# Kernel tuning notes

Measured on AMD Instinct MI355X. Metric: run time of the kernel, lower is better.

Reference implementation:

```python
import jax, jax.numpy as jnp
import numpy as np

MARGIN = 1.0
EPS = 1e-11


def setup_inputs() -> dict:
    key = jax.random.key(0)
    k1, k2, k3 = jax.random.split(key, 3)
    B, D, C = 8192, 512, 128
    features = jax.random.normal(k1, (B, D), dtype=jnp.float32)
    labels = jax.random.randint(k2, (B,), 0, C, dtype=jnp.int64)
    neg_u = jax.random.uniform(k3, (B,), dtype=jnp.float32)
    return {"features": features, "labels": labels, "neg_u": neg_u}


def reference(features, labels, neg_u):
    n = features.shape[0]
    sq = jnp.sum(features * features, axis=1)  # [n]
    d2 = sq[:, None] + sq[None, :] - 2.0 * (features @ features.T)
    dist = jnp.sqrt(jnp.clip(d2, EPS, None))  # [n, n]

    same = labels[:, None] == labels[None, :]
    eye = jnp.eye(n, dtype=bool)
    pos_mask = same & ~eye           # valid positives per anchor
    neg_mask = ~same                 # valid negatives per anchor
    n_neg = neg_mask.sum(axis=1)     # [n]

    # deterministic "random" negative: pick the floor(u * n_neg)-th negative
    # (stable argsort puts negatives first, preserving original order)
    order = jnp.argsort(jnp.where(neg_mask, 0, 1), axis=1, stable=True)  # [n, n]
    k = jnp.floor(neg_u * n_neg.astype(neg_u.dtype)).astype(jnp.int32)
    k = jnp.clip(k, 0, jnp.maximum(n_neg - 1, 0).astype(jnp.int32))
    neg_idx = jnp.take_along_axis(order, k[:, None], axis=1)[:, 0]       # [n]
    neg_dist = dist[jnp.arange(n), neg_idx]                               # [n]

    # MarginRankingLoss(y=1): max(0, margin + pos_dist - neg_dist), per (anchor, pos) pair
    valid = pos_mask & (n_neg > 0)[:, None]
    per_pair = jnp.maximum(MARGIN + dist - neg_dist[:, None], 0.0)
    counter = valid.sum()
    total = jnp.where(valid, per_pair, 0.0).sum()
    return total / counter.astype(total.dtype)
```

## Files before the change

kernel.cpp:

```cpp
#include <hip/hip_runtime.h>
#include <hip/hip_bf16.h>
#include <cstdint>

#define NN 8192
#define DD 512
#define NC 128

typedef unsigned short u16;
typedef __attribute__((ext_vector_type(8))) short short8;
typedef __attribute__((ext_vector_type(4))) float f32x4;

#define AS1 __attribute__((address_space(1)))
#define AS3 __attribute__((address_space(3)))

#define FB_OFF   ((size_t)0)
#define SQ_OFF   (FB_OFF + (size_t)NN*DD*2)
#define ND_OFF   (SQ_OFF + (size_t)NN*4)
#define ACC_OFF  (ND_OFF + (size_t)NN*4)
#define CC_OFF   (ACC_OFF + 64)
#define POS_OFF  (CC_OFF + 1024)

__global__ __launch_bounds__(256) void k_pos(const int* __restrict__ labels,
    int* __restrict__ cc, int* __restrict__ pos, int* __restrict__ accz) {
  const int c = blockIdx.x;
  const int wid = threadIdx.x >> 6, lane = threadIdx.x & 63;
  if (c == 0 && threadIdx.x < 16) accz[threadIdx.x] = 0;
  __shared__ int wcnt[4], woff[4];
  const int base0 = wid * 2048;
  int cw = 0;
  for (int b = 0; b < 2048; b += 64)
    cw += __popcll(__ballot(labels[base0 + b + lane] == c));
  if (lane == 0) wcnt[wid] = cw;
  __syncthreads();
  if (threadIdx.x == 0) {
    int o = 0;
    #pragma unroll
    for (int w = 0; w < 4; ++w) { woff[w] = o; o += wcnt[w]; }
    cc[c] = o;
  }
  __syncthreads();
  int off = woff[wid];
  for (int b = 0; b < 2048; b += 64) {
    const int idx = base0 + b + lane;
    const int hit = (labels[idx] == c);
    const unsigned long long m = __ballot(hit);
    if (hit) pos[c * 128 + off + __popcll(m & ((1ull << lane) - 1ull))] = idx;
    off += __popcll(m);
  }
  __syncthreads();
  const int nc = cc[c];
  for (int t = nc + threadIdx.x; t < 128; t += 256) pos[c * 128 + t] = 0;
}

__global__ __launch_bounds__(256) void k_pn(const float* __restrict__ F,
    const int* __restrict__ labels, const float* __restrict__ negu,
    const int* __restrict__ cc, const int* __restrict__ pos,
    u16* __restrict__ Fb, float* __restrict__ sq, float* __restrict__ nd) {
  const int wid = threadIdx.x >> 6, lane = threadIdx.x & 63;
  if (blockIdx.x < 2048) {
    const int row = blockIdx.x * 4 + wid;
    const float* fr = F + (size_t)row * DD + lane * 8;
    float4 v0 = *(const float4*)fr;
    float4 v1 = *(const float4*)(fr + 4);
    float s = v0.x*v0.x + v0.y*v0.y + v0.z*v0.z + v0.w*v0.w
            + v1.x*v1.x + v1.y*v1.y + v1.z*v1.z + v1.w*v1.w;
    #pragma unroll
    for (int o = 32; o; o >>= 1) s += __shfl_xor(s, o);
    float t[8] = {v0.x, v0.y, v0.z, v0.w, v1.x, v1.y, v1.z, v1.w};
    unsigned p[8];
    #pragma unroll
    for (int e = 0; e < 8; ++e) {
      unsigned b = __float_as_uint(t[e]);
      b += 0x7fffu + ((b >> 16) & 1u);
      p[e] = b >> 16;
    }
    uint4 w;
    w.x = p[0] | (p[1] << 16); w.y = p[2] | (p[3] << 16);
    w.z = p[4] | (p[5] << 16); w.w = p[6] | (p[7] << 16);
    *(uint4*)(Fb + (size_t)row * DD + lane * 8) = w;
    if (lane == 0) sq[row] = s;
  } else {
    const int i = (blockIdx.x - 2048) * 4 + wid;
    const int c = labels[i];
    const int nc = cc[c];
    const int n_neg = NN - nc;
    if (n_neg <= 0) { if (lane == 0) nd[i] = __builtin_inff(); return; }
    int k = (int)floorf(negu[i] * (float)n_neg);
    k = k < 0 ? 0 : (k > n_neg - 1 ? n_neg - 1 : k);
    const int* pc = pos + c * 128;
    const int p0 = pc[lane], p1 = pc[64 + lane];
    const int t = __popcll(__ballot((lane < nc) && (p0 - lane <= k)))
                + __popcll(__ballot((64 + lane < nc) && (p1 - (64 + lane) <= k)));
    const int j = k + t;
    const float* fi = F + (size_t)i * DD + lane * 8;
    const float* fj = F + (size_t)j * DD + lane * 8;
    float4 a0 = *(const float4*)fi, a1 = *(const float4*)(fi + 4);
    float4 b0 = *(const float4*)fj, b1 = *(const float4*)(fj + 4);
    float d  = a0.x*b0.x + a0.y*b0.y + a0.z*b0.z + a0.w*b0.w
             + a1.x*b1.x + a1.y*b1.y + a1.z*b1.z + a1.w*b1.w;
    float si = a0.x*a0.x + a0.y*a0.y + a0.z*a0.z + a0.w*a0.w
             + a1.x*a1.x + a1.y*a1.y + a1.z*a1.z + a1.w*a1.w;
    float sj = b0.x*b0.x + b0.y*b0.y + b0.z*b0.z + b0.w*b0.w
             + b1.x*b1.x + b1.y*b1.y + b1.z*b1.z + b1.w*b1.w;
    #pragma unroll
    for (int o = 32; o; o >>= 1) {
      d += __shfl_xor(d, o); si += __shfl_xor(si, o); sj += __shfl_xor(sj, o);
    }
    if (lane == 0) nd[i] = sqrtf(fmaxf(si + sj - 2.0f * d, 1e-11f));
  }
}

__global__ __launch_bounds__(256) void k_cls(const u16* __restrict__ Fb,
    const float* __restrict__ sq, const float* __restrict__ nd,
    const int* __restrict__ cc, const int* __restrict__ pos,
    float* __restrict__ accf, float* __restrict__ out) {
  const int c = blockIdx.x >> 1, half = blockIdx.x & 1;
  __shared__ __align__(16) u16 P[128 * 512];
  __shared__ int posc[128];
  __shared__ float red[4];
  const int tid = threadIdx.x, wid = tid >> 6, lane = tid & 63;
  const int nc = cc[c];
  if (tid < 128) posc[tid] = pos[c * 128 + tid];
  __syncthreads();
  if (nc >= 2 && half * 64 < nc) {
    const int wr = half, wc = wid;
    const int r16 = lane & 15, gg = lane >> 4;
    const char* fb = (const char*)Fb;

    #pragma unroll 8
    for (int s = 0; s < 32; ++s) {
      const int row = wid * 32 + s;
      const int gr = posc[row];
      __builtin_amdgcn_global_load_lds(
          (const AS1 void*)(fb + (size_t)gr * 1024 + ((lane ^ (s & 7)) << 4)),
          (AS3 void*)(&P[row * 512]), 16, 0, 0);
    }

    f32x4 acc[4][2];
    #pragma unroll
    for (int m = 0; m < 4; ++m)
      #pragma unroll
      for (int n = 0; n < 2; ++n)
        #pragma unroll
        for (int q = 0; q < 4; ++q) acc[m][n][q] = 0.0f;

    __syncthreads();
    #pragma unroll 4
    for (int t = 0; t < 16; ++t) {
      short8 af[4], bf[2];
      #pragma unroll
      for (int m = 0; m < 4; ++m) {
        const int row = wr * 64 + m * 16 + r16;
        const int gl = (t * 4 + gg) ^ (row & 7);
        af[m] = *(const short8*)&P[row * 512 + gl * 8];
      }
      #pragma unroll
      for (int n = 0; n < 2; ++n) {
        const int row = wc * 32 + n * 16 + r16;
        const int gl = (t * 4 + gg) ^ (row & 7);
        bf[n] = *(const short8*)&P[row * 512 + gl * 8];
      }
      #pragma unroll
      for (int m = 0; m < 4; ++m)
        #pragma unroll
        for (int n = 0; n < 2; ++n)
          acc[m][n] = __builtin_amdgcn_mfma_f32_16x16x32_bf16(af[m], bf[n], acc[m][n], 0, 0, 0);
    }

    float lsum = 0.0f;
    int njv[2]; float sqj[2];
    #pragma unroll
    for (int n = 0; n < 2; ++n) {
      const int nj = wc * 32 + n * 16 + r16;
      njv[n] = nj; sqj[n] = sq[posc[nj]];
    }
    #pragma unroll
    for (int m = 0; m < 4; ++m) {
      #pragma unroll
      for (int q = 0; q < 4; ++q) {
        const int mi = wr * 64 + m * 16 + gg * 4 + q;
        const int i = posc[mi];
        const float sqi = sq[i], ndi = nd[i];
        const bool vi = mi < nc;
        #pragma unroll
        for (int n = 0; n < 2; ++n) {
          const float g = acc[m][n][q];
          const float dist = sqrtf(fmaxf(sqi + sqj[n] - 2.0f * g, 1e-11f));
          if (vi & (njv[n] < nc) & (mi != njv[n]))
            lsum += fmaxf(1.0f + dist - ndi, 0.0f);
        }
      }
    }
    #pragma unroll
    for (int o = 32; o; o >>= 1) lsum += __shfl_xor(lsum, o);
    if (lane == 0) red[wid] = lsum;
    __syncthreads();
    if (tid == 0) atomicAdd(accf, red[0] + red[1] + red[2] + red[3]);
  }
  if (tid == 0) {
    int* cnt  = (int*)accf + 1;
    int* done = (int*)accf + 2;
    if (half == 0 && nc < NN) atomicAdd(cnt, nc * (nc - 1));
    __threadfence();
    if (atomicAdd(done, 1) == 2 * NC - 1) {
      const float tot = atomicAdd(accf, 0.0f);
      const int n = atomicAdd(cnt, 0);
      out[0] = tot / (float)n;
    }
  }
}

extern "C" void kernel_launch(void* const* d_in, const int* in_sizes, int n_in,
                              void* d_out, int out_size, void* d_ws, size_t ws_size,
                              hipStream_t stream) {
  const float* F = (const float*)d_in[0];
  const int* labels = (const int*)d_in[1];
  const float* negu = (const float*)d_in[2];
  char* ws = (char*)d_ws;
  u16*   Fb    = (u16*)(ws + FB_OFF);
  float* sq    = (float*)(ws + SQ_OFF);
  float* nd    = (float*)(ws + ND_OFF);
  float* accf  = (float*)(ws + ACC_OFF);
  int*   cc    = (int*)(ws + CC_OFF);
  int*   pos   = (int*)(ws + POS_OFF);

  k_pos<<<NC,     256, 0, stream>>>(labels, cc, pos, (int*)accf);
  k_pn <<<4096,   256, 0, stream>>>(F, labels, negu, cc, pos, Fb, sq, nd);
  k_cls<<<2 * NC, 256, 0, stream>>>(Fb, sq, nd, cc, pos, accf, (float*)d_out);
}
```

Before: 34.31 us.

## Fuse class-position bucketing into negative-distance kernel, dropping one launch

Removes the separate k_pos kernel and merges per-class bucketing into k_pn. Blocks 0..NC-1 now each build their class's position list in shared memory and compute the negative distances for all anchors of that class. The remaining 2048 blocks do the bf16 conversion and squared norms. This saves one kernel launch and its dependency gap. In exchange, negative-distance work drops from 2048 blocks to 128, and each of those blocks first runs a serial label scan before it can compute anything.

```diff
diff --git a/kernel.cpp b/kernel.cpp
--- a/kernel.cpp
+++ b/kernel.cpp
@@ -20,45 +20,13 @@
 #define CC_OFF   (ACC_OFF + 64)
 #define POS_OFF  (CC_OFF + 1024)
 
-__global__ __launch_bounds__(256) void k_pos(const int* __restrict__ labels,
-    int* __restrict__ cc, int* __restrict__ pos, int* __restrict__ accz) {
-  const int c = blockIdx.x;
-  const int wid = threadIdx.x >> 6, lane = threadIdx.x & 63;
-  if (c == 0 && threadIdx.x < 16) accz[threadIdx.x] = 0;
-  __shared__ int wcnt[4], woff[4];
-  const int base0 = wid * 2048;
-  int cw = 0;
-  for (int b = 0; b < 2048; b += 64)
-    cw += __popcll(__ballot(labels[base0 + b + lane] == c));
-  if (lane == 0) wcnt[wid] = cw;
-  __syncthreads();
-  if (threadIdx.x == 0) {
-    int o = 0;
-    #pragma unroll
-    for (int w = 0; w < 4; ++w) { woff[w] = o; o += wcnt[w]; }
-    cc[c] = o;
-  }
-  __syncthreads();
-  int off = woff[wid];
-  for (int b = 0; b < 2048; b += 64) {
-    const int idx = base0 + b + lane;
-    const int hit = (labels[idx] == c);
-    const unsigned long long m = __ballot(hit);
-    if (hit) pos[c * 128 + off + __popcll(m & ((1ull << lane) - 1ull))] = idx;
-    off += __popcll(m);
-  }
-  __syncthreads();
-  const int nc = cc[c];
-  for (int t = nc + threadIdx.x; t < 128; t += 256) pos[c * 128 + t] = 0;
-}
-
 __global__ __launch_bounds__(256) void k_pn(const float* __restrict__ F,
     const int* __restrict__ labels, const float* __restrict__ negu,
-    const int* __restrict__ cc, const int* __restrict__ pos,
-    u16* __restrict__ Fb, float* __restrict__ sq, float* __restrict__ nd) {
+    u16* __restrict__ Fb, float* __restrict__ sq, int* __restrict__ cc,
+    int* __restrict__ pos, float* __restrict__ nd, int* __restrict__ accz) {
   const int wid = threadIdx.x >> 6, lane = threadIdx.x & 63;
-  if (blockIdx.x < 2048) {
-    const int row = blockIdx.x * 4 + wid;
+  if (blockIdx.x >= NC) {
+    const int row = (blockIdx.x - NC) * 4 + wid;
     const float* fr = F + (size_t)row * DD + lane * 8;
     float4 v0 = *(const float4*)fr;
     float4 v1 = *(const float4*)(fr + 4);
@@ -80,33 +48,79 @@
     *(uint4*)(Fb + (size_t)row * DD + lane * 8) = w;
     if (lane == 0) sq[row] = s;
   } else {
-    const int i = (blockIdx.x - 2048) * 4 + wid;
-    const int c = labels[i];
-    const int nc = cc[c];
+    const int c = blockIdx.x;
+    if (c == 0 && threadIdx.x < 16) accz[threadIdx.x] = 0;
+    __shared__ int wcnt[4], woff[4], ncs;
+    __shared__ int posc[128], jm[128];
+    __shared__ float pd[128][4], psi[128][4], psj[128][4];
+    const int base0 = wid * 2048;
+    int cw = 0;
+    for (int b = 0; b < 2048; b += 64)
+      cw += __popcll(__ballot(labels[base0 + b + lane] == c));
+    if (lane == 0) wcnt[wid] = cw;
+    __syncthreads();
+    if (threadIdx.x == 0) {
+      int o = 0;
+      #pragma unroll
+      for (int w = 0; w < 4; ++w) { woff[w] = o; o += wcnt[w]; }
+      cc[c] = o; ncs = o;
+    }
+    __syncthreads();
+    int off = woff[wid];
+    for (int b = 0; b < 2048; b += 64) {
+      const int idx = base0 + b + lane;
+      const int hit = (labels[idx] == c);
+      const unsigned long long m = __ballot(hit);
+      if (hit) {
+        const int slot = off + __popcll(m & ((1ull << lane) - 1ull));
+        pos[c * 128 + slot] = idx;
+        posc[slot] = idx;
+      }
+      off += __popcll(m);
+    }
+    __syncthreads();
+    const int nc = ncs;
+    for (int t = nc + threadIdx.x; t < 128; t += 256) {
+      pos[c * 128 + t] = 0; posc[t] = 0;
+    }
+    __syncthreads();
     const int n_neg = NN - nc;
-    if (n_neg <= 0) { if (lane == 0) nd[i] = __builtin_inff(); return; }
-    int k = (int)floorf(negu[i] * (float)n_neg);
-    k = k < 0 ? 0 : (k > n_neg - 1 ? n_neg - 1 : k);
-    const int* pc = pos + c * 128;
-    const int p0 = pc[lane], p1 = pc[64 + lane];
-    const int t = __popcll(__ballot((lane < nc) && (p0 - lane <= k)))
-                + __popcll(__ballot((64 + lane < nc) && (p1 - (64 + lane) <= k)));
-    const int j = k + t;
-    const float* fi = F + (size_t)i * DD + lane * 8;
-    const float* fj = F + (size_t)j * DD + lane * 8;
-    float4 a0 = *(const float4*)fi, a1 = *(const float4*)(fi + 4);
-    float4 b0 = *(const float4*)fj, b1 = *(const float4*)(fj + 4);
-    float d  = a0.x*b0.x + a0.y*b0.y + a0.z*b0.z + a0.w*b0.w
-             + a1.x*b1.x + a1.y*b1.y + a1.z*b1.z + a1.w*b1.w;
-    float si = a0.x*a0.x + a0.y*a0.y + a0.z*a0.z + a0.w*a0.w
-             + a1.x*a1.x + a1.y*a1.y + a1.z*a1.z + a1.w*a1.w;
-    float sj = b0.x*b0.x + b0.y*b0.y + b0.z*b0.z + b0.w*b0.w
-             + b1.x*b1.x + b1.y*b1.y + b1.z*b1.z + b1.w*b1.w;
-    #pragma unroll
-    for (int o = 32; o; o >>= 1) {
-      d += __shfl_xor(d, o); si += __shfl_xor(si, o); sj += __shfl_xor(sj, o);
-    }
-    if (lane == 0) nd[i] = sqrtf(fmaxf(si + sj - 2.0f * d, 1e-11f));
+    if (n_neg <= 0) {
+      for (int m = threadIdx.x; m < nc; m += 256) nd[posc[m]] = __builtin_inff();
+      return;
+    }
+    const int p0 = posc[lane], p1 = posc[64 + lane];
+    for (int m = wid; m < nc; m += 4) {
+      const int i = posc[m];
+      int k = (int)floorf(negu[i] * (float)n_neg);
+      k = k < 0 ? 0 : (k > n_neg - 1 ? n_neg - 1 : k);
+      const int t = __popcll(__ballot((lane < nc) && (p0 - lane <= k)))
+                  + __popcll(__ballot((64 + lane < nc) && (p1 - (64 + lane) <= k)));
+      if (lane == 0) jm[m] = k + t;
+    }
+    __syncthreads();
+    const int mq = threadIdx.x >> 2, q = threadIdx.x & 3;
+    for (int m = mq; m < nc; m += 64) {
+      const float* fi = F + (size_t)posc[m] * DD + q * 128;
+      const float* fj = F + (size_t)jm[m]   * DD + q * 128;
+      float d = 0.0f, si = 0.0f, sj = 0.0f;
+      #pragma unroll 8
+      for (int e = 0; e < 32; ++e) {
+        const float4 a = ((const float4*)fi)[e];
+        const float4 b = ((const float4*)fj)[e];
+        d  += a.x*b.x + a.y*b.y + a.z*b.z + a.w*b.w;
+        si += a.x*a.x + a.y*a.y + a.z*a.z + a.w*a.w;
+        sj += b.x*b.x + b.y*b.y + b.z*b.z + b.w*b.w;
+      }
+      pd[m][q] = d; psi[m][q] = si; psj[m][q] = sj;
+    }
+    __syncthreads();
+    for (int m = threadIdx.x; m < nc; m += 256) {
+      const float d  = pd[m][0]  + pd[m][1]  + pd[m][2]  + pd[m][3];
+      const float si = psi[m][0] + psi[m][1] + psi[m][2] + psi[m][3];
+      const float sj = psj[m][0] + psj[m][1] + psj[m][2] + psj[m][3];
+      nd[posc[m]] = sqrtf(fmaxf(si + sj - 2.0f * d, 1e-11f));
+    }
   }
 }
 
@@ -224,7 +238,6 @@
   int*   cc    = (int*)(ws + CC_OFF);
   int*   pos   = (int*)(ws + POS_OFF);
 
-  k_pos<<<NC,     256, 0, stream>>>(labels, cc, pos, (int*)accf);
-  k_pn <<<4096,   256, 0, stream>>>(F, labels, negu, cc, pos, Fb, sq, nd);
-  k_cls<<<2 * NC, 256, 0, stream>>>(Fb, sq, nd, cc, pos, accf, (float*)d_out);
+  k_pn <<<NC + 2048, 256, 0, stream>>>(F, labels, negu, Fb, sq, cc, pos, nd, (int*)accf);
+  k_cls<<<2 * NC,    256, 0, stream>>>(Fb, sq, nd, cc, pos, accf, (float*)d_out);
 }
```

After: 45.38 us. 1.32x slower.
